# Performance work log

Measured on AMD Instinct MI355X. Metric: run time of the kernel, lower is better.

## Reference

```python
import jax, jax.numpy as jnp
import numpy as np

B, S, D, A = 16, 2048, 512, 512

def setup_inputs() -> dict:
    key = jax.random.key(0)
    ks = jax.random.split(key, 7)
    scale = 1.0 / np.sqrt(D)
    return {
        "query": jax.random.normal(ks[0], (B, S, D), dtype=jnp.float32),
        "key_": jax.random.normal(ks[1], (B, S, D), dtype=jnp.float32),
        "value": jax.random.normal(ks[2], (B, S, D), dtype=jnp.float32),
        "Wq": jax.random.normal(ks[3], (D, A), dtype=jnp.float32) * scale,
        "Wk": jax.random.normal(ks[4], (D, A), dtype=jnp.float32) * scale,
        "Wv": jax.random.normal(ks[5], (D, A), dtype=jnp.float32) * scale,
        "Ws": jax.random.normal(ks[6], (A, 1), dtype=jnp.float32) * (1.0 / np.sqrt(A)),
    }

def reference(query, key_, value, Wq, Wk, Wv, Ws):
    # Dense projections (no bias): [B,S,D] @ [D,A] -> [B,S,A]
    q = jnp.einsum("bsd,da->bsa", query, Wq)
    k = jnp.einsum("bsd,da->bsa", key_, Wk)
    v = jnp.einsum("bsd,da->bsa", value, Wv)
    # Additive (Bahdanau) scores: tanh(q+k) @ Ws -> [B,S]
    scores = jnp.einsum("bsa,a->bs", jnp.tanh(q + k), Ws[:, 0])
    attention_weights = jax.nn.softmax(scores, axis=1)[..., None]  # [B,S,1]
    context_vector = jnp.sum(attention_weights * v, axis=1)        # [B,A]
    return context_vector, attention_weights
```

## Files before the change

kernel.cpp:

```cpp
#include <hip/hip_runtime.h>
#include <hip/hip_bf16.h>
#include <stdint.h>

#define B_ 16
#define S_ 2048
#define D_ 512
#define A_ 512

typedef __attribute__((ext_vector_type(4))) float f32x4;
typedef __attribute__((ext_vector_type(8))) short bf16x8;

__device__ inline unsigned short f2bf(float f) {
  union { float f; unsigned int u; } c; c.f = f;
  unsigned int u = c.u;
  unsigned int r = (u + 0x7fffu + ((u >> 16) & 1u)) >> 16;
  return (unsigned short)r;
}

__device__ inline unsigned pk2bf(float x, float y) {
  __hip_bfloat162 p = __float22bfloat162_rn(float2{x, y});
  union { __hip_bfloat162 h; unsigned u; } c; c.h = p;
  return c.u;
}

__device__ inline float fast_tanh(float x) {
  float e = __expf(2.0f * x);
  return 1.0f - 2.0f * __builtin_amdgcn_rcpf(e + 1.0f);
}

__device__ inline void gload_lds16(const void* g, void* l) {
  __builtin_amdgcn_global_load_lds((const __attribute__((address_space(1))) void*)g,
                                   (__attribute__((address_space(3))) void*)l, 16, 0, 0);
}

__global__ __launch_bounds__(256) void k0_pack_w(const float* __restrict__ Wq,
                                                 const float* __restrict__ Wk,
                                                 unsigned short* __restrict__ WT) {
  __shared__ unsigned short tile[64][65];
  int bid = blockIdx.x;
  int dt = bid & 15, at = bid >> 4;
  int d0 = dt * 64, a0 = at * 64;
  int t = threadIdx.x;
  int col = t & 63, rbase = t >> 6;
#pragma unroll
  for (int r8 = 0; r8 < 16; ++r8) {
    int row = r8 * 4 + rbase;
    int dcat = d0 + row;
    float f = (dcat < 512) ? Wq[(size_t)dcat * 512 + a0 + col]
                           : Wk[(size_t)(dcat - 512) * 512 + a0 + col];
    tile[row][col] = f2bf(f);
  }
  __syncthreads();
#pragma unroll
  for (int r8 = 0; r8 < 16; ++r8) {
    int arow = r8 * 4 + rbase;
    WT[(size_t)(a0 + arow) * 1024 + d0 + col] = tile[col][arow];
  }
}

__global__ __launch_bounds__(512, 2) void k1_scores(
    const float* __restrict__ Q, const float* __restrict__ K,
    const unsigned short* __restrict__ WT, const float* __restrict__ Wsv,
    float* __restrict__ score) {
  __shared__ unsigned short Al[2][128 * 32];
  __shared__ unsigned short Bl[2][512 * 32];

  const int t = threadIdx.x;
  const int lane = t & 63, w = t >> 6;
  const int frow = lane & 15, fsl = lane >> 4;
  const int row0 = (int)blockIdx.x * 128;

  const int ar = t >> 2, ak = (t & 3) * 8;
  const int abyte = ar * 64 + (((t & 3) ^ ((ar >> 1) & 3)) * 16);

  float4 rA0[2], rA1[2];

  auto issueA = [&](int p, float4* r) {
    const float* src = (p < 16) ? Q : K;
    const float* ap = src + (size_t)(row0 + ar) * 512 + ((p * 32) & 511) + ak;
    r[0] = *(const float4*)(ap);
    r[1] = *(const float4*)(ap + 4);
  };
  auto writeA = [&](const float4* r, int buf) {
    uint4 d;
    d.x = pk2bf(r[0].x, r[0].y);
    d.y = pk2bf(r[0].z, r[0].w);
    d.z = pk2bf(r[1].x, r[1].y);
    d.w = pk2bf(r[1].z, r[1].w);
    *(uint4*)((char*)&Al[buf][0] + abyte) = d;
  };
  auto stageB = [&](int p, int buf) {
#pragma unroll
    for (int q = 0; q < 4; ++q) {
      int pc = (w * 4 + q) * 64 + lane;
      int row = pc >> 2;
      int sl = (pc & 3) ^ ((row >> 1) & 3);
      const char* g = (const char*)WT + (size_t)row * 2048 + p * 64 + sl * 16;
      gload_lds16(g, (char*)&Bl[buf][0] + (size_t)(w * 4 + q) * 1024);
    }
  };

  f32x4 acc[8][4];
#pragma unroll
  for (int m = 0; m < 8; ++m)
#pragma unroll
    for (int n = 0; n < 4; ++n) acc[m][n] = (f32x4){0.f, 0.f, 0.f, 0.f};

  const int ch = (fsl ^ ((frow >> 1) & 3)) * 16;

  auto doMfma = [&](int CUR) {
    bf16x8 af[8], bfr[4];
#pragma unroll
    for (int m = 0; m < 8; ++m)
      af[m] = *(const bf16x8*)((const char*)&Al[CUR][0] + (m * 16 + frow) * 64 + ch);
#pragma unroll
    for (int n = 0; n < 4; ++n)
      bfr[n] = *(const bf16x8*)((const char*)&Bl[CUR][0] + (w * 64 + n * 16 + frow) * 64 + ch);
    __builtin_amdgcn_s_setprio(1);
#pragma unroll
    for (int m = 0; m < 8; ++m)
#pragma unroll
      for (int n = 0; n < 4; ++n)
        acc[m][n] = __builtin_amdgcn_mfma_f32_16x16x32_bf16(af[m], bfr[n], acc[m][n], 0, 0, 0);
    __builtin_amdgcn_s_setprio(0);
  };

  issueA(0, rA0);
  stageB(0, 0);
  __builtin_amdgcn_sched_barrier(0);
  issueA(1, rA1);
  writeA(rA0, 0);
  asm volatile("s_waitcnt vmcnt(2) lgkmcnt(0)" ::: "memory");
  __builtin_amdgcn_s_barrier();

  auto phase = [&](int p, int CUR, float4* rCur, const float4* rNext) {
    stageB(p + 1, CUR ^ 1);
    __builtin_amdgcn_sched_barrier(0);
    issueA(p + 2, rCur);
    doMfma(CUR);
    writeA(rNext, CUR ^ 1);
    asm volatile("s_waitcnt vmcnt(2) lgkmcnt(0)" ::: "memory");
    __builtin_amdgcn_s_barrier();
  };

  for (int kt2 = 0; kt2 < 15; ++kt2) {
    phase(2 * kt2 + 0, 0, rA0, rA1);
    phase(2 * kt2 + 1, 1, rA1, rA0);
  }

  stageB(31, 1);
  doMfma(0);
  writeA(rA1, 1);
  asm volatile("s_waitcnt vmcnt(0) lgkmcnt(0)" ::: "memory");
  __builtin_amdgcn_s_barrier();
  doMfma(1);

  float wsv[4];
#pragma unroll
  for (int n = 0; n < 4; ++n) wsv[n] = Wsv[w * 64 + n * 16 + frow];
  __syncthreads();
  float* scw = (float*)&Al[0][0];
#pragma unroll
  for (int m = 0; m < 8; ++m) {
#pragma unroll
    for (int ii = 0; ii < 4; ++ii) {
      float s = 0.f;
#pragma unroll
      for (int n = 0; n < 4; ++n)
        s += fast_tanh(acc[m][n][ii]) * wsv[n];
      s += __shfl_xor(s, 1);
      s += __shfl_xor(s, 2);
      s += __shfl_xor(s, 4);
      s += __shfl_xor(s, 8);
      if (frow == 0) scw[w * 128 + m * 16 + fsl * 4 + ii] = s;
    }
  }
  __syncthreads();
  if (t < 128) {
    float s = 0.f;
#pragma unroll
    for (int ww = 0; ww < 8; ++ww) s += scw[ww * 128 + t];
    score[row0 + t] = s;
  }
}

__global__ __launch_bounds__(256) void k3_vsum(const float* __restrict__ value,
                                               const float* __restrict__ score,
                                               float* __restrict__ upart,
                                               float* __restrict__ outw) {
  int bid = blockIdx.x;
  int dh = bid & 1, sc = (bid >> 1) & 15, b = bid >> 5;
  int t = threadIdx.x;
  int lane = t & 63, wave = t >> 6;
  int dg = t & 63, sg = t >> 6;
  __shared__ float red[4], red2[4];
  __shared__ float wl[128];
  __shared__ f32x4 redv[4][64];

  float v[8];
  float mx = -1e30f;
#pragma unroll
  for (int e = 0; e < 8; ++e) {
    float p = score[(size_t)b * S_ + e * 256 + t];
    v[e] = p;
    mx = fmaxf(mx, p);
  }
  for (int off = 1; off < 64; off <<= 1) mx = fmaxf(mx, __shfl_xor(mx, off));
  if (lane == 0) red[wave] = mx;
  __syncthreads();
  mx = fmaxf(fmaxf(red[0], red[1]), fmaxf(red[2], red[3]));
  float sum = 0.f;
#pragma unroll
  for (int e = 0; e < 8; ++e) sum += expf(v[e] - mx);
  for (int off = 1; off < 64; off <<= 1) sum += __shfl_xor(sum, off);
  if (lane == 0) red2[wave] = sum;
  __syncthreads();
  sum = red2[0] + red2[1] + red2[2] + red2[3];
  float inv = 1.f / sum;

  int s0 = sc * 128;
  if (t < 128) {
    float ww = expf(score[(size_t)b * S_ + s0 + t] - mx) * inv;
    wl[t] = ww;
    if (dh == 0) outw[(size_t)b * S_ + s0 + t] = ww;
  }
  __syncthreads();

  const float* vp = value + ((size_t)b * S_ + s0) * 512 + dh * 256 + dg * 4;
  f32x4 a = (f32x4){0.f, 0.f, 0.f, 0.f};
  for (int s = sg; s < 128; s += 4) {
    float4 v4 = *(const float4*)(vp + (size_t)s * 512);
    float ws = wl[s];
    a[0] += ws * v4.x; a[1] += ws * v4.y; a[2] += ws * v4.z; a[3] += ws * v4.w;
  }
  redv[sg][dg] = a;
  __syncthreads();
  if (sg == 0) {
    f32x4 r = redv[0][dg] + redv[1][dg] + redv[2][dg] + redv[3][dg];
    float* dst = upart + (size_t)(sc * 16 + b) * 512 + dh * 256 + dg * 4;
    dst[0] = r[0]; dst[1] = r[1]; dst[2] = r[2]; dst[3] = r[3];
  }
}

__global__ __launch_bounds__(512) void k4_ctx(const float* __restrict__ upart,
                                              const float* __restrict__ Wv,
                                              float* __restrict__ out) {
  int b = blockIdx.x, t = threadIdx.x;
  __shared__ float ul[512];
  float u = 0.f;
#pragma unroll
  for (int c = 0; c < 16; ++c) u += upart[(size_t)(c * 16 + b) * 512 + t];
  ul[t] = u;
  __syncthreads();
  float acc = 0.f;
#pragma unroll 8
  for (int d = 0; d < 512; ++d) acc += ul[d] * Wv[(size_t)d * 512 + t];
  out[(size_t)b * 512 + t] = acc;
}

extern "C" void kernel_launch(void* const* d_in, const int* in_sizes, int n_in,
                              void* d_out, int out_size, void* d_ws, size_t ws_size,
                              hipStream_t stream) {
  const float* Q  = (const float*)d_in[0];
  const float* Kk = (const float*)d_in[1];
  const float* V  = (const float*)d_in[2];
  const float* Wq = (const float*)d_in[3];
  const float* Wk = (const float*)d_in[4];
  const float* Wv = (const float*)d_in[5];
  const float* Ws = (const float*)d_in[6];
  float* out = (float*)d_out;

  char* ws = (char*)d_ws;
  unsigned short* WT = (unsigned short*)ws;
  float* score = (float*)(ws + (1 << 20));
  float* upart = (float*)(ws + (1 << 20) + (512 << 10));

  float* outw = out + B_ * A_;

  k0_pack_w<<<dim3(128), dim3(256), 0, stream>>>(Wq, Wk, WT);
  k1_scores<<<dim3(256), dim3(512), 0, stream>>>(Q, Kk, WT, Ws, score);
  k3_vsum<<<dim3(512), dim3(256), 0, stream>>>(V, score, upart, outw);
  k4_ctx<<<dim3(16), dim3(512), 0, stream>>>(upart, Wv, out);
}
```

Before: 96.29 us.

## Replace hand-tuned waitcnt barriers with syncthreads and split ctx kernel across more blocks

The GEMM pipeline's explicit sched_barrier, partial vmcnt waits and raw s_barrier are replaced by plain __syncthreads, and the first writeA now comes before issuing the next A load. The final context kernel goes from 16 blocks of 512 threads to 64 blocks of 256 threads, each handling 128 columns with a two-way split over d. Both changes simplify the code. The syncthreads version likely waits for all outstanding global loads (vmcnt(0)), which would remove the prefetch overlap. The wider k4 grid is meant to raise parallelism in the small GEMV tail.

After: 88.01 us. -8.6%, faster.

```diff
diff --git a/kernel.cpp b/kernel.cpp
--- a/kernel.cpp
+++ b/kernel.cpp
@@ -127,20 +127,16 @@
 
   issueA(0, rA0);
   stageB(0, 0);
-  __builtin_amdgcn_sched_barrier(0);
+  writeA(rA0, 0);
   issueA(1, rA1);
-  writeA(rA0, 0);
-  asm volatile("s_waitcnt vmcnt(2) lgkmcnt(0)" ::: "memory");
-  __builtin_amdgcn_s_barrier();
+  __syncthreads();
 
   auto phase = [&](int p, int CUR, float4* rCur, const float4* rNext) {
     stageB(p + 1, CUR ^ 1);
-    __builtin_amdgcn_sched_barrier(0);
     issueA(p + 2, rCur);
     doMfma(CUR);
     writeA(rNext, CUR ^ 1);
-    asm volatile("s_waitcnt vmcnt(2) lgkmcnt(0)" ::: "memory");
-    __builtin_amdgcn_s_barrier();
+    __syncthreads();
   };
 
   for (int kt2 = 0; kt2 < 15; ++kt2) {
@@ -151,8 +147,7 @@
   stageB(31, 1);
   doMfma(0);
   writeA(rA1, 1);
-  asm volatile("s_waitcnt vmcnt(0) lgkmcnt(0)" ::: "memory");
-  __builtin_amdgcn_s_barrier();
+  __syncthreads();
   doMfma(1);
 
   float wsv[4];
@@ -220,9 +215,10 @@
 
   int s0 = sc * 128;
   if (t < 128) {
-    float ww = expf(score[(size_t)b * S_ + s0 + t] - mx) * inv;
+    size_t o = (size_t)b * S_ + s0 + t;
+    float ww = expf(score[o] - mx) * inv;
     wl[t] = ww;
-    if (dh == 0) outw[(size_t)b * S_ + s0 + t] = ww;
+    if (dh == 0) outw[o] = ww;
   }
   __syncthreads();
 
@@ -242,20 +238,29 @@
   }
 }
 
-__global__ __launch_bounds__(512) void k4_ctx(const float* __restrict__ upart,
+__global__ __launch_bounds__(256) void k4_ctx(const float* __restrict__ upart,
                                               const float* __restrict__ Wv,
                                               float* __restrict__ out) {
-  int b = blockIdx.x, t = threadIdx.x;
+  int b = blockIdx.x >> 2, q = blockIdx.x & 3;
+  int t = threadIdx.x;
+  int col = q * 128 + (t & 127), dhf = t >> 7;
   __shared__ float ul[512];
-  float u = 0.f;
-#pragma unroll
-  for (int c = 0; c < 16; ++c) u += upart[(size_t)(c * 16 + b) * 512 + t];
-  ul[t] = u;
+  __shared__ float part[2][128];
+  for (int i = t; i < 512; i += 256) {
+    float u = 0.f;
+#pragma unroll
+    for (int c = 0; c < 16; ++c) u += upart[(size_t)(c * 16 + b) * 512 + i];
+    ul[i] = u;
+  }
   __syncthreads();
   float acc = 0.f;
 #pragma unroll 8
-  for (int d = 0; d < 512; ++d) acc += ul[d] * Wv[(size_t)d * 512 + t];
-  out[(size_t)b * 512 + t] = acc;
+  for (int d = dhf * 256; d < dhf * 256 + 256; ++d)
+    acc += ul[d] * Wv[(size_t)d * 512 + col];
+  part[dhf][t & 127] = acc;
+  __syncthreads();
+  if (dhf == 0)
+    out[(size_t)b * 512 + col] = part[0][t & 127] + part[1][t & 127];
 }
 
 extern "C" void kernel_launch(void* const* d_in, const int* in_sizes, int n_in,
@@ -280,5 +285,5 @@
   k0_pack_w<<<dim3(128), dim3(256), 0, stream>>>(Wq, Wk, WT);
   k1_scores<<<dim3(256), dim3(512), 0, stream>>>(Q, Kk, WT, Ws, score);
   k3_vsum<<<dim3(512), dim3(256), 0, stream>>>(V, score, upart, outw);
-  k4_ctx<<<dim3(16), dim3(512), 0, stream>>>(upart, Wv, out);
-}
+  k4_ctx<<<dim3(64), dim3(256), 0, stream>>>(upart, Wv, out);
+}
```
